# Kernel optimization log

Hardware: AMD Instinct MI355X
Metric: run time of the kernel (lower is better)

The kernel has to match this reference:

```python
import jax, jax.numpy as jnp
import numpy as np

PAD = 0
NEG_INF = -1e30

B, P, Q, D = 32, 4096, 64, 128  # batch, passage len, question len, nhid


def setup_inputs() -> dict:
    key = jax.random.key(0)
    k1, k2, k3, k4, k5, k6 = jax.random.split(key, 6)
    return {
        "tensor_H": jax.random.normal(k1, (B, P, D), dtype=jnp.float32),
        "tensor_U": jax.random.normal(k2, (B, Q, D), dtype=jnp.float32),
        "M": jax.random.normal(k3, (B, P, D), dtype=jnp.float32),
        "sentence_word_rep": jax.random.randint(k4, (B, P), 0, 10000, dtype=jnp.int64),
        "W_attn": jax.random.normal(k5, (D, D), dtype=jnp.float32) / np.sqrt(D),
        "W_cls": jax.random.normal(k6, (5 * D, 2), dtype=jnp.float32) / np.sqrt(5 * D),
    }


def reference(tensor_H, tensor_U, M, sentence_word_rep, W_attn, W_cls):
    # Matrix attention (bilinear): S[b,p,q] = h_p^T W u_q  -> (B, P, Q)
    S = jnp.einsum("bpd,de,bqe->bpq", tensor_H, W_attn, tensor_U)
    # context-to-query: softmax over question axis, then bmm with U
    c2q = jnp.einsum("bpq,bqd->bpd", jax.nn.softmax(S, axis=2), tensor_U)
    # query-to-context: softmax over passage axis of row-max, weighted sum of H
    b_attn = jax.nn.softmax(jnp.max(S, axis=2), axis=-1)        # (B, P)
    q2c = jnp.einsum("bp,bpd->bd", b_attn, tensor_H)[:, None, :]  # (B, 1, D) broadcast over P
    # G = [H; c2q; H*c2q; H*q2c] -> (B, P, 4D); G_M = [G; M] -> (B, P, 5D)
    G_M = jnp.concatenate(
        [tensor_H, c2q, tensor_H * c2q, tensor_H * q2c, M], axis=2
    )
    # masked max-pool over passage positions (mask where token == PAD)
    pad_mask = (sentence_word_rep == PAD)[:, :, None]           # (B, P, 1)
    pooled = jnp.max(jnp.where(pad_mask, NEG_INF, G_M), axis=1)  # (B, 5D)
    # final linear classifier (no bias)
    return pooled @ W_cls                                        # (B, 2)
```

## Files before the change

### kernel.cpp

```cpp
#include <hip/hip_runtime.h>

#define B_ 32
#define P_ 4096
#define Q_ 64
#define D_ 128

#define PART_STRIDE 772
#define NCHUNK 32
#define CHUNK_ROWS 128
#define TWS_BYTES (96*16384)

typedef __attribute__((ext_vector_type(8))) short bf16x8;
typedef __attribute__((ext_vector_type(4))) float f32x4;

__device__ __forceinline__ unsigned int asu(float x) { return __float_as_uint(x); }
__device__ __forceinline__ float asf(unsigned int x) { return __uint_as_float(x); }

__global__ __launch_bounds__(256) void k_T(const float* __restrict__ U,
                                           const float* __restrict__ W,
                                           char* __restrict__ Tws) {
  __shared__ float Wl[128*132];
  __shared__ float Ul[8*128];
  const int b = blockIdx.x >> 3, qc = blockIdx.x & 7;
  const int t = threadIdx.x;
#pragma unroll
  for (int k = 0; k < 16; ++k) {
    int i = t*4 + k*1024;
    float4 wv = *(const float4*)(W + i);
    int d = i >> 7, e = i & 127;
    *(float4*)(&Wl[d*132 + e]) = wv;
  }
  {
    int i = t*4;
    int q = i >> 7, e = i & 127;
    *(float4*)(&Ul[q*128 + e]) =
        *(const float4*)(U + ((size_t)(b*Q_ + qc*8 + q))*D_ + e);
  }
  __syncthreads();
  const int d = t & 127, qhalf = t >> 7;
  char* Thi = Tws + b*16384;
  char* Tlo = Tws + 32*16384 + b*16384;
  char* Utl = Tws + 64*16384 + b*16384;
#pragma unroll
  for (int pass = 0; pass < 4; ++pass) {
    const int ql = pass*2 + qhalf;
    const int qg = qc*8 + ql;
    float acc = 0.f;
#pragma unroll
    for (int e = 0; e < 128; e += 4) {
      float4 wv = *(float4*)(&Wl[d*132 + e]);
      float4 uv = *(float4*)(&Ul[ql*128 + e]);
      acc += wv.x*uv.x + wv.y*uv.y + wv.z*uv.z + wv.w*uv.w;
    }
    unsigned int au = asu(acc);
    unsigned short hs = (unsigned short)(au >> 16);
    float lo = acc - asf(au & 0xFFFF0000u);
    unsigned short ls = (unsigned short)(asu(lo) >> 16);
    int ta = (qg*256 + 2*d) ^ ((qg & 7) << 4);
    *(unsigned short*)(Thi + ta) = hs;
    *(unsigned short*)(Tlo + ta) = ls;
    float uval = Ul[ql*128 + d];
    int ua = (d*128 + 2*qg) ^ ((d & 7) << 4);
    *(unsigned short*)(Utl + ua) = (unsigned short)(asu(uval) >> 16);
  }
}

__global__ __launch_bounds__(512, 4) void k_main(
    const float* __restrict__ H, const float* __restrict__ M,
    const int* __restrict__ tok, const char* __restrict__ Tws,
    float* __restrict__ part) {
  __shared__ __align__(16) char Tl[32768];
  __shared__ __align__(16) char Pl[16384];
  __shared__ __align__(16) float mrow[128];
  __shared__ __align__(16) float rzrow[128];
  __shared__ __align__(16) float prow[128];
  __shared__ __align__(16) float bm[128];
  __shared__ int tkl[128];

  const int bid = blockIdx.x;
  const int b = bid >> 5, chunk = bid & 31;
  const int t = threadIdx.x, wv = t >> 6, l = t & 63;
  const int r15 = l & 15, g4 = l >> 4;
  const char* Thi_g = Tws + b*16384;
  const char* Tlo_g = Tws + 32*16384 + b*16384;
  const char* Utl   = Tws + 64*16384 + b*16384;

  const int dd = wv*16 + r15;
  bf16x8 bu0 = *(const bf16x8*)(Utl + ((dd*128 +  0 + g4*16) ^ ((dd & 7) << 4)));
  bf16x8 bu1 = *(const bf16x8*)(Utl + ((dd*128 + 64 + g4*16) ^ ((dd & 7) << 4)));

  {
    const uint4* sh = (const uint4*)Thi_g;
    const uint4* sl = (const uint4*)Tlo_g;
    uint4* dh = (uint4*)Tl;
    uint4* dl = (uint4*)(Tl + 16384);
    dh[t]       = sh[t];
    dh[t + 512] = sh[t + 512];
    dl[t]       = sl[t];
    dl[t + 512] = sl[t + 512];
  }
  if (t < 128) tkl[t] = tok[b*P_ + chunk*CHUNK_ROWS + t];
  __syncthreads();

  const int rowB = b*P_ + chunk*CHUNK_ROWS;

  {
    const int lrow0 = wv*16;
    const float* Arow = H + (size_t)(rowB + lrow0 + r15)*D_;
    f32x4 fA[4], fB[4];
#pragma unroll
    for (int ks = 0; ks < 4; ++ks) {
      const float* ap = Arow + ks*32 + g4*8;
      fA[ks] = *(const f32x4*)(ap);
      fB[ks] = *(const f32x4*)(ap + 4);
    }
    union { bf16x8 v; unsigned int u[4]; } Ah[4], Al[4];
#pragma unroll
    for (int ks = 0; ks < 4; ++ks) {
      unsigned int a0 = asu(fA[ks][0]), a1 = asu(fA[ks][1]),
                   a2 = asu(fA[ks][2]), a3 = asu(fA[ks][3]);
      unsigned int c0 = asu(fB[ks][0]), c1 = asu(fB[ks][1]),
                   c2 = asu(fB[ks][2]), c3 = asu(fB[ks][3]);
      Ah[ks].u[0] = (a1 & 0xFFFF0000u) | (a0 >> 16);
      Ah[ks].u[1] = (a3 & 0xFFFF0000u) | (a2 >> 16);
      Ah[ks].u[2] = (c1 & 0xFFFF0000u) | (c0 >> 16);
      Ah[ks].u[3] = (c3 & 0xFFFF0000u) | (c2 >> 16);
      float p0 = fA[ks][0] - asf(a0 & 0xFFFF0000u);
      float p1 = fA[ks][1] - asf(a1 & 0xFFFF0000u);
      float p2 = fA[ks][2] - asf(a2 & 0xFFFF0000u);
      float p3 = fA[ks][3] - asf(a3 & 0xFFFF0000u);
      float p4 = fB[ks][0] - asf(c0 & 0xFFFF0000u);
      float p5 = fB[ks][1] - asf(c1 & 0xFFFF0000u);
      float p6 = fB[ks][2] - asf(c2 & 0xFFFF0000u);
      float p7 = fB[ks][3] - asf(c3 & 0xFFFF0000u);
      Al[ks].u[0] = (asu(p1) & 0xFFFF0000u) | (asu(p0) >> 16);
      Al[ks].u[1] = (asu(p3) & 0xFFFF0000u) | (asu(p2) >> 16);
      Al[ks].u[2] = (asu(p5) & 0xFFFF0000u) | (asu(p4) >> 16);
      Al[ks].u[3] = (asu(p7) & 0xFFFF0000u) | (asu(p6) >> 16);
    }
    f32x4 sacc[4];
#pragma unroll
    for (int qt = 0; qt < 4; ++qt) sacc[qt] = (f32x4){0.f, 0.f, 0.f, 0.f};
#pragma unroll
    for (int ks = 0; ks < 4; ++ks) {
#pragma unroll
      for (int qt = 0; qt < 4; ++qt) {
        int q = qt*16 + r15;
        int off = (q*256 + ks*64 + g4*16) ^ ((q & 7) << 4);
        bf16x8 bh = *(const bf16x8*)(Tl + off);
        bf16x8 bl = *(const bf16x8*)(Tl + 16384 + off);
        sacc[qt] = __builtin_amdgcn_mfma_f32_16x16x32_bf16(Al[ks].v, bh, sacc[qt], 0, 0, 0);
        sacc[qt] = __builtin_amdgcn_mfma_f32_16x16x32_bf16(Ah[ks].v, bl, sacc[qt], 0, 0, 0);
        sacc[qt] = __builtin_amdgcn_mfma_f32_16x16x32_bf16(Ah[ks].v, bh, sacc[qt], 0, 0, 0);
      }
    }
    float m[4];
#pragma unroll
    for (int j = 0; j < 4; ++j)
      m[j] = fmaxf(fmaxf(sacc[0][j], sacc[1][j]), fmaxf(sacc[2][j], sacc[3][j]));
#pragma unroll
    for (int off = 1; off <= 8; off <<= 1)
#pragma unroll
      for (int j = 0; j < 4; ++j) m[j] = fmaxf(m[j], __shfl_xor(m[j], off));
    float Zp[4] = {0.f, 0.f, 0.f, 0.f};
#pragma unroll
    for (int qt = 0; qt < 4; ++qt)
#pragma unroll
      for (int j = 0; j < 4; ++j) {
        float e = __expf(sacc[qt][j] - m[j]);
        Zp[j] += e;
        int p = lrow0 + g4*4 + j, q = qt*16 + r15;
        int off = (p*128 + 2*q) ^ ((p & 7) << 4);
        *(unsigned short*)(Pl + off) = (unsigned short)(asu(e) >> 16);
      }
#pragma unroll
    for (int off = 1; off <= 8; off <<= 1)
#pragma unroll
      for (int j = 0; j < 4; ++j) Zp[j] += __shfl_xor(Zp[j], off);
    if (r15 == 0) {
#pragma unroll
      for (int j = 0; j < 4; ++j) {
        mrow[lrow0 + g4*4 + j]  = m[j];
        rzrow[lrow0 + g4*4 + j] = __builtin_amdgcn_rcpf(Zp[j]);
      }
    }
  }
  __syncthreads();

  float m0 = mrow[l], m1 = mrow[l + 64];
  float Lm = fmaxf(m0, m1);
#pragma unroll
  for (int off = 1; off <= 32; off <<= 1) Lm = fmaxf(Lm, __shfl_xor(Lm, off));
  float ssum = __expf(m0 - Lm) + __expf(m1 - Lm);
#pragma unroll
  for (int off = 1; off <= 32; off <<= 1) ssum += __shfl_xor(ssum, off);
  if (t < 128) {
    prow[t] = __expf(mrow[t] - Lm);
    bm[t]   = tkl[t] ? 0.f : -1.0e38f;
  }
  __syncthreads();

  float hb[8][4], mb[8][4];
#pragma unroll
  for (int rti = 0; rti < 8; ++rti) {
    const int rt = (rti + wv) & 7;
    const float* Hrow = H + (size_t)(rowB + rt*16 + g4*4)*D_ + dd;
    const float* Mrow = M + (size_t)(rowB + rt*16 + g4*4)*D_ + dd;
#pragma unroll
    for (int j = 0; j < 4; ++j) {
      hb[rti][j] = Hrow[(size_t)j*D_];
      mb[rti][j] = Mrow[(size_t)j*D_];
    }
  }

  float v = 0.f, xH = -3.0e38f, nH = 3.0e38f;
  float xC = -3.0e38f, xHC = -3.0e38f, xM = -3.0e38f;
#pragma unroll
  for (int rti = 0; rti < 8; ++rti) {
    const int rt = (rti + wv) & 7;
    f32x4 pv = (f32x4){0.f, 0.f, 0.f, 0.f};
    {
      int pr0 = rt*16 + r15;
      bf16x8 a0 = *(bf16x8*)(Pl + ((pr0*128 +  0 + g4*16) ^ ((r15 & 7) << 4)));
      bf16x8 a1 = *(bf16x8*)(Pl + ((pr0*128 + 64 + g4*16) ^ ((r15 & 7) << 4)));
      pv = __builtin_amdgcn_mfma_f32_16x16x32_bf16(a0, bu0, pv, 0, 0, 0);
      pv = __builtin_amdgcn_mfma_f32_16x16x32_bf16(a1, bu1, pv, 0, 0, 0);
    }
    const int rg = rt*16 + g4*4;
    f32x4 prw = *(const f32x4*)&prow[rg];
    f32x4 rzw = *(const f32x4*)&rzrow[rg];
    f32x4 bmw = *(const f32x4*)&bm[rg];
#pragma unroll
    for (int j = 0; j < 4; ++j) {
      const float bmax = bmw[j];
      const float bmin = -bmax;
      float h  = hb[rti][j];
      float mv = mb[rti][j];
      float c  = pv[j] * rzw[j];
      v   += prw[j]*h;
      xH   = fmaxf(xH,  h + bmax);
      nH   = fminf(nH,  h + bmin);
      xC   = fmaxf(xC,  c + bmax);
      xHC  = fmaxf(xHC, h*c + bmax);
      xM   = fmaxf(xM,  mv + bmax);
    }
  }
#pragma unroll
  for (int off = 16; off <= 32; off <<= 1) {
    v   += __shfl_xor(v, off);
    xH   = fmaxf(xH,  __shfl_xor(xH,  off));
    nH   = fminf(nH,  __shfl_xor(nH,  off));
    xC   = fmaxf(xC,  __shfl_xor(xC,  off));
    xHC  = fmaxf(xHC, __shfl_xor(xHC, off));
    xM   = fmaxf(xM,  __shfl_xor(xM,  off));
  }
  float* pp = part + (size_t)bid*PART_STRIDE;
  if (t == 0) { pp[0] = Lm; pp[1] = ssum; }
  if (g4 == 0) {
    pp[2 + dd]   = v;
    pp[130 + dd] = xH;
    pp[258 + dd] = nH;
    pp[386 + dd] = xC;
    pp[514 + dd] = xHC;
    pp[642 + dd] = xM;
  }
}

__global__ __launch_bounds__(128) void k_final(const float* __restrict__ part,
                                               const float* __restrict__ Wc,
                                               float* __restrict__ out) {
  __shared__ float pooled[640];
  __shared__ float r0s[2], r1s[2];
  const int b = blockIdx.x, t = threadIdx.x;
  const float* pb = part + (size_t)b*NCHUNK*PART_STRIDE;
  float L = -3.0e38f;
#pragma unroll
  for (int c = 0; c < NCHUNK; ++c) L = fmaxf(L, pb[c*PART_STRIDE]);
  float S = 0.f, V = 0.f;
  float mh = -3.0e38f, nh = 3.0e38f, mc = -3.0e38f, mhc = -3.0e38f, mm = -3.0e38f;
#pragma unroll
  for (int c = 0; c < NCHUNK; ++c) {
    const float* p = pb + c*PART_STRIDE;
    float e = __expf(p[0] - L);
    S += p[1]*e;
    V += p[2 + t]*e;
    mh  = fmaxf(mh,  p[130 + t]);
    nh  = fminf(nh,  p[258 + t]);
    mc  = fmaxf(mc,  p[386 + t]);
    mhc = fmaxf(mhc, p[514 + t]);
    mm  = fmaxf(mm,  p[642 + t]);
  }
  float q2c = V / S;
  pooled[t]       = mh;
  pooled[128 + t] = mc;
  pooled[256 + t] = mhc;
  pooled[384 + t] = (q2c >= 0.f) ? q2c*mh : q2c*nh;
  pooled[512 + t] = mm;
  __syncthreads();
  float a0 = 0.f, a1 = 0.f;
#pragma unroll
  for (int k = t; k < 640; k += 128) {
    float pv = pooled[k];
    a0 += pv*Wc[k*2 + 0];
    a1 += pv*Wc[k*2 + 1];
  }
#pragma unroll
  for (int off = 32; off; off >>= 1) {
    a0 += __shfl_xor(a0, off);
    a1 += __shfl_xor(a1, off);
  }
  if ((t & 63) == 0) { r0s[t >> 6] = a0; r1s[t >> 6] = a1; }
  __syncthreads();
  if (t == 0) {
    out[b*2 + 0] = r0s[0] + r0s[1];
    out[b*2 + 1] = r1s[0] + r1s[1];
  }
}

extern "C" void kernel_launch(void* const* d_in, const int* in_sizes, int n_in,
                              void* d_out, int out_size, void* d_ws, size_t ws_size,
                              hipStream_t stream) {
  const float* H   = (const float*)d_in[0];
  const float* U   = (const float*)d_in[1];
  const float* M   = (const float*)d_in[2];
  const int*   tok = (const int*)d_in[3];
  const float* Wa  = (const float*)d_in[4];
  const float* Wc  = (const float*)d_in[5];
  float* out = (float*)d_out;
  char* wsc = (char*)d_ws;
  char* Tws = wsc;
  float* part = (float*)(wsc + TWS_BYTES);

  hipLaunchKernelGGL(k_T,     dim3(256),        dim3(256), 0, stream, U, Wa, Tws);
  hipLaunchKernelGGL(k_main,  dim3(B_*NCHUNK),  dim3(512), 0, stream, H, M, tok, Tws, part);
  hipLaunchKernelGGL(k_final, dim3(B_),         dim3(128), 0, stream, part, Wc, out);
}
```

Measured before the change: 53.00 us.

## Transpose epilogue MFMA so H/M loads become row-contiguous float4

Swaps the MFMA operand order in the c2q epilogue so each lane holds four consecutive feature columns of one passage row instead of four rows of one column. H and M can then be read as contiguous float4 vectors per row and interleaved with the MFMA loop, rather than preloaded as 64 strided scalars per thread. Because each lane now covers one row, the cross-lane reduction changes from two shuffle steps to four steps over four-wide vectors. The occupancy hint drops from 4 to 3 blocks per CU, which lets the compiler use more registers.

After: 58.89 us. 1.11x slower.

```diff
diff --git a/kernel.cpp b/kernel.cpp
--- a/kernel.cpp
+++ b/kernel.cpp
@@ -65,7 +65,7 @@
   }
 }
 
-__global__ __launch_bounds__(512, 4) void k_main(
+__global__ __launch_bounds__(512, 3) void k_main(
     const float* __restrict__ H, const float* __restrict__ M,
     const int* __restrict__ tok, const char* __restrict__ Tws,
     float* __restrict__ part) {
@@ -85,9 +85,9 @@
   const char* Tlo_g = Tws + 32*16384 + b*16384;
   const char* Utl   = Tws + 64*16384 + b*16384;
 
-  const int dd = wv*16 + r15;
-  bf16x8 bu0 = *(const bf16x8*)(Utl + ((dd*128 +  0 + g4*16) ^ ((dd & 7) << 4)));
-  bf16x8 bu1 = *(const bf16x8*)(Utl + ((dd*128 + 64 + g4*16) ^ ((dd & 7) << 4)));
+  const int dA = wv*16 + r15;
+  bf16x8 au0 = *(const bf16x8*)(Utl + ((dA*128 + g4*16 +  0) ^ ((dA & 7) << 4)));
+  bf16x8 au1 = *(const bf16x8*)(Utl + ((dA*128 + g4*16 + 64) ^ ((dA & 7) << 4)));
 
   {
     const uint4* sh = (const uint4*)Thi_g;
@@ -200,69 +200,61 @@
   }
   __syncthreads();
 
-  float hb[8][4], mb[8][4];
+  f32x4 v4  = (f32x4){0.f, 0.f, 0.f, 0.f};
+  f32x4 xH4 = (f32x4){-3.0e38f, -3.0e38f, -3.0e38f, -3.0e38f};
+  f32x4 nH4 = (f32x4){ 3.0e38f,  3.0e38f,  3.0e38f,  3.0e38f};
+  f32x4 xC4 = (f32x4){-3.0e38f, -3.0e38f, -3.0e38f, -3.0e38f};
+  f32x4 xHC4= (f32x4){-3.0e38f, -3.0e38f, -3.0e38f, -3.0e38f};
+  f32x4 xM4 = (f32x4){-3.0e38f, -3.0e38f, -3.0e38f, -3.0e38f};
+  const int dbase = wv*16 + g4*4;
 #pragma unroll
   for (int rti = 0; rti < 8; ++rti) {
     const int rt = (rti + wv) & 7;
-    const float* Hrow = H + (size_t)(rowB + rt*16 + g4*4)*D_ + dd;
-    const float* Mrow = M + (size_t)(rowB + rt*16 + g4*4)*D_ + dd;
+    const int p = rt*16 + r15;
+    const int pswz = (p & 7) << 4;
+    bf16x8 pb0 = *(bf16x8*)(Pl + ((p*128 + g4*16 +  0) ^ pswz));
+    bf16x8 pb1 = *(bf16x8*)(Pl + ((p*128 + g4*16 + 64) ^ pswz));
+    f32x4 pv = (f32x4){0.f, 0.f, 0.f, 0.f};
+    pv = __builtin_amdgcn_mfma_f32_16x16x32_bf16(au0, pb0, pv, 0, 0, 0);
+    pv = __builtin_amdgcn_mfma_f32_16x16x32_bf16(au1, pb1, pv, 0, 0, 0);
+    const float prw = prow[p], rz = rzrow[p], bmv = bm[p];
+    f32x4 h4 = *(const f32x4*)(H + (size_t)(rowB + p)*D_ + dbase);
+    f32x4 m4 = *(const f32x4*)(M + (size_t)(rowB + p)*D_ + dbase);
 #pragma unroll
     for (int j = 0; j < 4; ++j) {
-      hb[rti][j] = Hrow[(size_t)j*D_];
-      mb[rti][j] = Mrow[(size_t)j*D_];
-    }
-  }
-
-  float v = 0.f, xH = -3.0e38f, nH = 3.0e38f;
-  float xC = -3.0e38f, xHC = -3.0e38f, xM = -3.0e38f;
-#pragma unroll
-  for (int rti = 0; rti < 8; ++rti) {
-    const int rt = (rti + wv) & 7;
-    f32x4 pv = (f32x4){0.f, 0.f, 0.f, 0.f};
-    {
-      int pr0 = rt*16 + r15;
-      bf16x8 a0 = *(bf16x8*)(Pl + ((pr0*128 +  0 + g4*16) ^ ((r15 & 7) << 4)));
-      bf16x8 a1 = *(bf16x8*)(Pl + ((pr0*128 + 64 + g4*16) ^ ((r15 & 7) << 4)));
-      pv = __builtin_amdgcn_mfma_f32_16x16x32_bf16(a0, bu0, pv, 0, 0, 0);
-      pv = __builtin_amdgcn_mfma_f32_16x16x32_bf16(a1, bu1, pv, 0, 0, 0);
-    }
-    const int rg = rt*16 + g4*4;
-    f32x4 prw = *(const f32x4*)&prow[rg];
-    f32x4 rzw = *(const f32x4*)&rzrow[rg];
-    f32x4 bmw = *(const f32x4*)&bm[rg];
+      float c = pv[j] * rz;
+      v4[j]   += prw*h4[j];
+      xH4[j]   = fmaxf(xH4[j],  h4[j] + bmv);
+      nH4[j]   = fminf(nH4[j],  h4[j] - bmv);
+      xC4[j]   = fmaxf(xC4[j],  c + bmv);
+      xHC4[j]  = fmaxf(xHC4[j], h4[j]*c + bmv);
+      xM4[j]   = fmaxf(xM4[j],  m4[j] + bmv);
+    }
+  }
+#pragma unroll
+  for (int off = 1; off <= 8; off <<= 1) {
 #pragma unroll
     for (int j = 0; j < 4; ++j) {
-      const float bmax = bmw[j];
-      const float bmin = -bmax;
-      float h  = hb[rti][j];
-      float mv = mb[rti][j];
-      float c  = pv[j] * rzw[j];
-      v   += prw[j]*h;
-      xH   = fmaxf(xH,  h + bmax);
-      nH   = fminf(nH,  h + bmin);
-      xC   = fmaxf(xC,  c + bmax);
-      xHC  = fmaxf(xHC, h*c + bmax);
-      xM   = fmaxf(xM,  mv + bmax);
-    }
-  }
-#pragma unroll
-  for (int off = 16; off <= 32; off <<= 1) {
-    v   += __shfl_xor(v, off);
-    xH   = fmaxf(xH,  __shfl_xor(xH,  off));
-    nH   = fminf(nH,  __shfl_xor(nH,  off));
-    xC   = fmaxf(xC,  __shfl_xor(xC,  off));
-    xHC  = fmaxf(xHC, __shfl_xor(xHC, off));
-    xM   = fmaxf(xM,  __shfl_xor(xM,  off));
+      v4[j]  += __shfl_xor(v4[j], off);
+      xH4[j]  = fmaxf(xH4[j],  __shfl_xor(xH4[j],  off));
+      nH4[j]  = fminf(nH4[j],  __shfl_xor(nH4[j],  off));
+      xC4[j]  = fmaxf(xC4[j],  __shfl_xor(xC4[j],  off));
+      xHC4[j] = fmaxf(xHC4[j], __shfl_xor(xHC4[j], off));
+      xM4[j]  = fmaxf(xM4[j],  __shfl_xor(xM4[j],  off));
+    }
   }
   float* pp = part + (size_t)bid*PART_STRIDE;
   if (t == 0) { pp[0] = Lm; pp[1] = ssum; }
-  if (g4 == 0) {
-    pp[2 + dd]   = v;
-    pp[130 + dd] = xH;
-    pp[258 + dd] = nH;
-    pp[386 + dd] = xC;
-    pp[514 + dd] = xHC;
-    pp[642 + dd] = xM;
+  if (r15 == 0) {
+#pragma unroll
+    for (int j = 0; j < 4; ++j) {
+      pp[2 + dbase + j]   = v4[j];
+      pp[130 + dbase + j] = xH4[j];
+      pp[258 + dbase + j] = nH4[j];
+      pp[386 + dbase + j] = xC4[j];
+      pp[514 + dbase + j] = xHC4[j];
+      pp[642 + dbase + j] = xM4[j];
+    }
   }
 }
 
```
